# Kernel tuning notes

Measured on AMD Instinct MI355X. Metric: run time of the kernel, lower is better.

The kernel has to match this reference:

```python
import jax, jax.numpy as jnp
import numpy as np


def _patch_points(P):
    # replicates: meshgrid(y,x,z, indexing='ij'); points = cat([zz, yy, xx], -1).reshape(-1,3)
    lin = jnp.linspace(-1.0, 1.0, P)
    a, b, c = jnp.meshgrid(lin, lin, lin, indexing='ij')  # all identical linspaces
    pts = jnp.stack([c, b, a], axis=-1).reshape(-1, 3)     # (P^3, 3)
    return pts


def _proj_locations(points, angles):
    # Tomographic projection geometry (generate_projections_location):
    # rotate points about the detector-vertical axis and keep in-plane coords.
    # points: (N,3); angles: (A,) radians. Returns (A, N, 2) grid coords (x, y)
    # in grid_sample convention (last dim: x indexes width, y indexes height).
    p0 = points[:, 0]
    p1 = points[:, 1]
    p2 = points[:, 2]
    c = jnp.cos(angles)[:, None]   # (A,1)
    s = jnp.sin(angles)[:, None]
    gx = p0[None, :] * c + p2[None, :] * s          # (A, N)
    gy = jnp.broadcast_to(p1[None, :], gx.shape)    # (A, N)
    return jnp.stack([gx, gy], axis=-1)             # (A, N, 2)


def _bilinear_sample(img, grid):
    # img: (C,H,W); grid: (N,2) in [-1,1], align_corners=True, padding zeros.
    C, H, W = img.shape
    ix = (grid[:, 0] + 1.0) * 0.5 * (W - 1)
    iy = (grid[:, 1] + 1.0) * 0.5 * (H - 1)
    ix0 = jnp.floor(ix)
    iy0 = jnp.floor(iy)
    ix1 = ix0 + 1.0
    iy1 = iy0 + 1.0
    wx1 = ix - ix0
    wx0 = 1.0 - wx1
    wy1 = iy - iy0
    wy0 = 1.0 - wy1

    def corner(iyc, ixc, w):
        valid = (ixc >= 0) & (ixc <= W - 1) & (iyc >= 0) & (iyc <= H - 1)
        xi = jnp.clip(ixc, 0, W - 1).astype(jnp.int32)
        yi = jnp.clip(iyc, 0, H - 1).astype(jnp.int32)
        return img[:, yi, xi] * (w * valid)[None, :]   # (C,N)

    return (corner(iy0, ix0, wy0 * wx0) + corner(iy0, ix1, wy0 * wx1)
            + corner(iy1, ix0, wy1 * wx0) + corner(iy1, ix1, wy1 * wx1))


def setup_inputs() -> dict:
    key = jax.random.key(0)
    k1, k2 = jax.random.split(key)
    B, A, P = 128, 121, 33
    x = jax.random.normal(k1, (B, A, P, P), dtype=jnp.float32)
    angles = jax.random.uniform(k2, (1, A), dtype=jnp.float32,
                                minval=0.0, maxval=2.0 * np.pi)
    return {"x": x, "angles": angles}


def reference(x, angles):
    B, A, P, _ = x.shape
    pts = _patch_points(P)                       # (P^3, 3)
    grids = _proj_locations(pts, angles[0])      # (A, P^3, 2)
    xs = jnp.transpose(x, (1, 0, 2, 3))          # (A, B, P, P)

    def body(acc, inp):
        xi, gi = inp                             # (B,P,P), (P^3,2)
        return acc + _bilinear_sample(xi, gi), None

    acc0 = jnp.zeros((B, P * P * P), dtype=x.dtype)
    acc, _ = jax.lax.scan(body, acc0, (xs, grids))
    x_fbp = acc.reshape(B, P, P, P) / A
    return x_fbp
```

## Files before the change

### kernel.cpp

```cpp
#include <hip/hip_runtime.h>
#include <hip/hip_fp16.h>
#include <math.h>


#define PDIM 33
#define PP   1089
#define A_   121
#define ROWW 47
#define PADL 7
#define BLK  384
#define NV   3
#define GRID 1280

typedef _Float16 h2v __attribute__((ext_vector_type(2)));

#if defined(__has_builtin)
#if __has_builtin(__builtin_amdgcn_fractf)
#define FRACTF(x) __builtin_amdgcn_fractf(x)
#endif
#endif
#ifndef FRACTF
#define FRACTF(x) ((x) - floorf(x))
#endif

__global__ void cs_kernel(const float* __restrict__ angles,
                          float2* __restrict__ csw, int A)
{
    int j = threadIdx.x;
    if (j < A) {
        float s, c;
        sincosf(angles[j], &s, &c);
        csw[j] = make_float2(c, s);
    }
}

__device__ __forceinline__ float fdot2u(unsigned int a, unsigned int b, float c)
{
    return __builtin_amdgcn_fdot2(__builtin_bit_cast(h2v, a),
                                  __builtin_bit_cast(h2v, b), c, false);
}

__global__ __launch_bounds__(BLK)
void fbp_adjoint_kernel(const float* __restrict__ x,
                        const float2* __restrict__ csw,
                        const float* __restrict__ angles,
                        float* __restrict__ out,
                        int nslice, float invA)
{
    __shared__ unsigned int dr[A_ * ROWW];
    __shared__ float2       cs_lds[A_];

    const int t = threadIdx.x;
    const bool use_ws = (csw != nullptr);
    if (!use_ws) {
        for (int j = t; j < A_; j += BLK) {
            float s, c;
            sincosf(angles[j], &s, &c);
            cs_lds[j] = make_float2(c, s);
        }
    }

    float u0[NV], u2[NV];
#pragma unroll
    for (int nn = 0; nn < NV; ++nn) {
        int n  = t + nn * BLK;
        int nc = (n < PP) ? n : (PP - 1);
        int q0 = nc / PDIM;
        int q2 = nc - q0 * PDIM;
        u0[nn] = (float)(q0 - 16);
        u2[nn] = (float)(q2 - 16);
    }

    for (int slice = blockIdx.x; slice < nslice; slice += GRID) {
        if (slice != (int)blockIdx.x) __syncthreads();

        const int hb = slice / PDIM;
        const int i1 = slice - hb * PDIM;
        const int b0 = 2 * hb;

        const float* r0 = x + (size_t)b0 * (A_ * PP) + (size_t)i1 * PDIM;
        const float* r1 = r0 + (size_t)(A_ * PP);
        for (int e = t; e < A_ * ROWW; e += BLK) {
            int j = e / ROWW;
            int p = e - j * ROWW;
            int k = p - PADL;
            float f0 = 0.0f, f1 = 0.0f;
            if (k >= 0 && k < PDIM) {
                size_t o = (size_t)j * PP + k;
                f0 = r0[o];
                f1 = r1[o];
            }
            dr[e] = __builtin_bit_cast(unsigned int,
                        __halves2half2(__float2half_rn(f0), __float2half_rn(f1)));
        }
        __syncthreads();

        float a0[NV] = {0.0f, 0.0f, 0.0f};
        float a1[NV] = {0.0f, 0.0f, 0.0f};

#pragma unroll 2
        for (int j = 0; j < A_; ++j) {
            float2 cj = use_ws ? csw[j] : cs_lds[j];
            const unsigned int* base = &dr[j * ROWW];
#pragma unroll
            for (int nn = 0; nn < NV; ++nn) {
                float ixp = fmaf(u2[nn], cj.x, fmaf(u0[nn], cj.y, 23.0f));
                int   kp  = (int)ixp;
                float w1  = FRACTF(ixp);
                unsigned int wp = __builtin_bit_cast(unsigned int,
                                    __builtin_amdgcn_cvt_pkrtz(1.0f - w1, w1));
                unsigned int d0 = base[kp];
                unsigned int d1 = base[kp + 1];
                unsigned int p0 = __builtin_amdgcn_perm(d1, d0, 0x05040100u);
                unsigned int p1 = __builtin_amdgcn_perm(d1, d0, 0x07060302u);
                a0[nn] = fdot2u(p0, wp, a0[nn]);
                a1[nn] = fdot2u(p1, wp, a1[nn]);
            }
        }

        float* ob0 = out + (size_t)b0 * (PDIM * PP) + (size_t)i1 * PDIM;
        float* ob1 = ob0 + (size_t)(PDIM * PP);
#pragma unroll
        for (int nn = 0; nn < NV; ++nn) {
            int n = t + nn * BLK;
            if (n < PP) {
                int q0 = n / PDIM;
                int q2 = n - q0 * PDIM;
                size_t o = (size_t)q0 * PP + q2;
                ob0[o] = a0[nn] * invA;
                ob1[o] = a1[nn] * invA;
            }
        }
    }
}

extern "C" void kernel_launch(void* const* d_in, const int* in_sizes, int n_in,
                              void* d_out, int out_size, void* d_ws, size_t ws_size,
                              hipStream_t stream)
{
    const float* x      = (const float*)d_in[0];
    const float* angles = (const float*)d_in[1];
    float* out          = (float*)d_out;

    const int A = in_sizes[1];
    const int B = in_sizes[0] / (A * PP);
    const int nslice = (B / 2) * PDIM;

    float2* csw = nullptr;
    if (ws_size >= sizeof(float2) * (size_t)A) {
        csw = (float2*)d_ws;
        cs_kernel<<<1, 128, 0, stream>>>(angles, csw, A);
    }

    dim3 grid(GRID < nslice ? GRID : nslice);
    dim3 block(BLK);
    fbp_adjoint_kernel<<<grid, block, 0, stream>>>(x, csw, angles, out,
                                                   nslice, 1.0f / (float)A);
}
```

Baseline: 215.3 us.

## Recast backprojection as sparse-weight fp16 GEMM on MFMA units

Builds a dense fp16 interpolation-weight matrix W (output voxel × angle·detector) from the angles, transposes and converts the input into an fp16 Xt matrix, and computes the backprojection as a W·Xtᵀ GEMM using 16x16x32 MFMA instructions. This replaces the per-voxel gather and dot2 loop with matrix-core work. The weight matrix is about 96% zeros, so far more FLOPs are issued, and two extra preprocessing kernels plus workspace traffic are added. The gather kernel remains as a fallback when the workspace is too small or the shapes differ.

New measurement: 239.0 us. +11.0%, slower.

```diff
diff --git a/kernel.cpp b/kernel.cpp
--- a/kernel.cpp
+++ b/kernel.cpp
@@ -6,6 +6,140 @@
 #define PDIM 33
 #define PP   1089
 #define A_   121
+#define K_   3993
+#define KP   4032
+#define MP   1152
+#define BM   128
+#define BN   128
+#define BK   32
+#define LDW  40
+#define MT   9
+#define NT   33
+#define OUTB 35937
+
+typedef _Float16 f16x8 __attribute__((ext_vector_type(8)));
+typedef float    f32x4 __attribute__((ext_vector_type(4)));
+
+
+__global__ __launch_bounds__(128)
+void wfill_kernel(const float* __restrict__ angles, __half* __restrict__ W)
+{
+    const int n = blockIdx.x;
+    const int t = threadIdx.x;
+    __half* row = W + (size_t)n * KP;
+    for (int e = t; e < KP; e += 128) row[e] = __float2half_rn(0.0f);
+    __syncthreads();
+    if (n >= PP || t >= A_) return;
+    const int j  = t;
+    const int i0 = n / PDIM;
+    const int i2 = n - i0 * PDIM;
+    float s, c;
+    sincosf(angles[j], &s, &c);
+    float ix = fmaf((float)(i2 - 16), c, fmaf((float)(i0 - 16), s, 16.0f));
+    float fl = floorf(ix);
+    int   k0 = (int)fl;
+    float w1 = ix - fl;
+    float w0 = 1.0f - w1;
+    __half* seg = row + j * PDIM;
+    if (k0 >= 0     && k0 < PDIM)     seg[k0]     = __float2half_rn(w0);
+    if (k0 + 1 >= 0 && k0 + 1 < PDIM) seg[k0 + 1] = __float2half_rn(w1);
+}
+
+__global__ __launch_bounds__(256)
+void xt_kernel(const float* __restrict__ x, __half* __restrict__ Xt)
+{
+    const int n  = blockIdx.x;
+    const int i1 = n >> 7;
+    const int b  = n & 127;
+    const float* src = x + (size_t)b * (A_ * PP) + (size_t)i1 * PDIM;
+    __half* dst = Xt + (size_t)n * KP;
+    for (int e = threadIdx.x; e < KP; e += 256) {
+        float v = 0.0f;
+        if (e < K_) {
+            int j = e / PDIM;
+            int k = e - j * PDIM;
+            v = src[(size_t)j * PP + k];
+        }
+        dst[e] = __float2half_rn(v);
+    }
+}
+
+__global__ __launch_bounds__(256)
+void gemm_kernel(const __half* __restrict__ W, const __half* __restrict__ Xt,
+                 float* __restrict__ out, float invA)
+{
+    __shared__ _Float16 As[BM * LDW];
+    __shared__ _Float16 Bs[BN * LDW];
+
+    const int tileM = blockIdx.x % MT;
+    const int tileN = blockIdx.x / MT;
+    const int t     = threadIdx.x;
+    const int lane  = t & 63;
+    const int wave  = t >> 6;
+    const int warpM = wave >> 1;
+    const int warpN = wave & 1;
+    const int quad  = lane >> 4;
+    const int l15   = lane & 15;
+
+    f32x4 acc[4][4] = {};
+
+    const __half* Abase = W  + (size_t)(tileM * BM) * KP;
+    const __half* Bbase = Xt + (size_t)(tileN * BN) * KP;
+
+    for (int kb = 0; kb < KP; kb += BK) {
+        __syncthreads();
+#pragma unroll
+        for (int i = 0; i < 2; ++i) {
+            int cidx = t + i * 256;
+            int row  = cidx >> 2;
+            int seg  = cidx & 3;
+            *(f16x8*)&As[row * LDW + seg * 8] =
+                *(const f16x8*)(Abase + (size_t)row * KP + kb + seg * 8);
+            *(f16x8*)&Bs[row * LDW + seg * 8] =
+                *(const f16x8*)(Bbase + (size_t)row * KP + kb + seg * 8);
+        }
+        __syncthreads();
+
+        f16x8 af[4], bf[4];
+#pragma unroll
+        for (int msub = 0; msub < 4; ++msub) {
+            int m = warpM * 64 + msub * 16 + l15;
+            af[msub] = *(const f16x8*)&As[m * LDW + quad * 8];
+        }
+#pragma unroll
+        for (int nsub = 0; nsub < 4; ++nsub) {
+            int n = warpN * 64 + nsub * 16 + l15;
+            bf[nsub] = *(const f16x8*)&Bs[n * LDW + quad * 8];
+        }
+#pragma unroll
+        for (int msub = 0; msub < 4; ++msub)
+#pragma unroll
+            for (int nsub = 0; nsub < 4; ++nsub)
+                acc[msub][nsub] = __builtin_amdgcn_mfma_f32_16x16x32_f16(
+                    af[msub], bf[nsub], acc[msub][nsub], 0, 0, 0);
+    }
+
+    const int i1 = tileN;
+#pragma unroll
+    for (int nsub = 0; nsub < 4; ++nsub) {
+        int bcol = warpN * 64 + nsub * 16 + l15;
+        float* ob = out + (size_t)bcol * OUTB + (size_t)i1 * PDIM;
+#pragma unroll
+        for (int msub = 0; msub < 4; ++msub) {
+#pragma unroll
+            for (int r = 0; r < 4; ++r) {
+                int m = tileM * BM + warpM * 64 + msub * 16 + quad * 4 + r;
+                if (m < PP) {
+                    int i0 = m / PDIM;
+                    int i2 = m - i0 * PDIM;
+                    ob[(size_t)i0 * PP + i2] = acc[msub][nsub][r] * invA;
+                }
+            }
+        }
+    }
+}
+
+
 #define ROWW 47
 #define PADL 7
 #define BLK  384
@@ -23,17 +157,6 @@
 #define FRACTF(x) ((x) - floorf(x))
 #endif
 
-__global__ void cs_kernel(const float* __restrict__ angles,
-                          float2* __restrict__ csw, int A)
-{
-    int j = threadIdx.x;
-    if (j < A) {
-        float s, c;
-        sincosf(angles[j], &s, &c);
-        csw[j] = make_float2(c, s);
-    }
-}
-
 __device__ __forceinline__ float fdot2u(unsigned int a, unsigned int b, float c)
 {
     return __builtin_amdgcn_fdot2(__builtin_bit_cast(h2v, a),
@@ -42,7 +165,6 @@
 
 __global__ __launch_bounds__(BLK)
 void fbp_adjoint_kernel(const float* __restrict__ x,
-                        const float2* __restrict__ csw,
                         const float* __restrict__ angles,
                         float* __restrict__ out,
                         int nslice, float invA)
@@ -51,13 +173,10 @@
     __shared__ float2       cs_lds[A_];
 
     const int t = threadIdx.x;
-    const bool use_ws = (csw != nullptr);
-    if (!use_ws) {
-        for (int j = t; j < A_; j += BLK) {
-            float s, c;
-            sincosf(angles[j], &s, &c);
-            cs_lds[j] = make_float2(c, s);
-        }
+    for (int j = t; j < A_; j += BLK) {
+        float s, c;
+        sincosf(angles[j], &s, &c);
+        cs_lds[j] = make_float2(c, s);
     }
 
     float u0[NV], u2[NV];
@@ -73,11 +192,9 @@
 
     for (int slice = blockIdx.x; slice < nslice; slice += GRID) {
         if (slice != (int)blockIdx.x) __syncthreads();
-
         const int hb = slice / PDIM;
         const int i1 = slice - hb * PDIM;
         const int b0 = 2 * hb;
-
         const float* r0 = x + (size_t)b0 * (A_ * PP) + (size_t)i1 * PDIM;
         const float* r1 = r0 + (size_t)(A_ * PP);
         for (int e = t; e < A_ * ROWW; e += BLK) {
@@ -97,10 +214,9 @@
 
         float a0[NV] = {0.0f, 0.0f, 0.0f};
         float a1[NV] = {0.0f, 0.0f, 0.0f};
-
 #pragma unroll 2
         for (int j = 0; j < A_; ++j) {
-            float2 cj = use_ws ? csw[j] : cs_lds[j];
+            float2 cj = cs_lds[j];
             const unsigned int* base = &dr[j * ROWW];
 #pragma unroll
             for (int nn = 0; nn < NV; ++nn) {
@@ -118,8 +234,8 @@
             }
         }
 
-        float* ob0 = out + (size_t)b0 * (PDIM * PP) + (size_t)i1 * PDIM;
-        float* ob1 = ob0 + (size_t)(PDIM * PP);
+        float* ob0 = out + (size_t)b0 * OUTB + (size_t)i1 * PDIM;
+        float* ob1 = ob0 + (size_t)OUTB;
 #pragma unroll
         for (int nn = 0; nn < NV; ++nn) {
             int n = t + nn * BLK;
@@ -134,6 +250,7 @@
     }
 }
 
+
 extern "C" void kernel_launch(void* const* d_in, const int* in_sizes, int n_in,
                               void* d_out, int out_size, void* d_ws, size_t ws_size,
                               hipStream_t stream)
@@ -144,16 +261,21 @@
 
     const int A = in_sizes[1];
     const int B = in_sizes[0] / (A * PP);
-    const int nslice = (B / 2) * PDIM;
-
-    float2* csw = nullptr;
-    if (ws_size >= sizeof(float2) * (size_t)A) {
-        csw = (float2*)d_ws;
-        cs_kernel<<<1, 128, 0, stream>>>(angles, csw, A);
-    }
-
-    dim3 grid(GRID < nslice ? GRID : nslice);
-    dim3 block(BLK);
-    fbp_adjoint_kernel<<<grid, block, 0, stream>>>(x, csw, angles, out,
-                                                   nslice, 1.0f / (float)A);
-}
+    const float invA = 1.0f / (float)A;
+
+    const size_t wBytes  = (size_t)MP * KP * sizeof(__half);
+    const size_t xtBytes = (size_t)(PDIM * B) * KP * sizeof(__half);
+
+    if (ws_size >= wBytes + xtBytes && A == A_ && B == 128) {
+        __half* W  = (__half*)d_ws;
+        __half* Xt = (__half*)((char*)d_ws + wBytes);
+        wfill_kernel<<<MP, 128, 0, stream>>>(angles, W);
+        xt_kernel<<<PDIM * B, 256, 0, stream>>>(x, Xt);
+        gemm_kernel<<<MT * NT, 256, 0, stream>>>(W, Xt, out, invA);
+    } else {
+        const int nslice = (B / 2) * PDIM;
+        dim3 grid(GRID < nslice ? GRID : nslice);
+        fbp_adjoint_kernel<<<grid, BLK, 0, stream>>>(x, angles, out,
+                                                     nslice, invA);
+    }
+}
```
